# Performance work log

Measured on AMD Instinct MI355X. Metric: run time of the kernel, lower is better.

Reference implementation:

```python
import jax, jax.numpy as jnp
import numpy as np

EPS = 1e-5

def _ln(x):
    m = jnp.mean(x, axis=-1, keepdims=True)
    v = jnp.mean((x - m) ** 2, axis=-1, keepdims=True)
    return (x - m) / jnp.sqrt(v + EPS)

def setup_inputs() -> dict:
    key = jax.random.key(0)
    ks = jax.random.split(key, 6)
    B, S, E, H = 2, 2048, 1024, 16
    sd = 1.0 / np.sqrt(E)
    x = jax.random.normal(ks[0], (B, S, E), dtype=jnp.float32)
    w_in = jax.random.normal(ks[1], (3 * E, E), dtype=jnp.float32) * sd
    w_out = jax.random.normal(ks[2], (E, E), dtype=jnp.float32) * sd
    w_fc = jax.random.normal(ks[3], (4 * E, E), dtype=jnp.float32) * sd
    b_fc = jnp.zeros((4 * E,), dtype=jnp.float32)
    w_proj = jax.random.normal(ks[4], (E, 4 * E), dtype=jnp.float32) * (1.0 / np.sqrt(4 * E))
    b_proj = jnp.zeros((E,), dtype=jnp.float32)
    return {"x": x, "w_in": w_in, "w_out": w_out, "w_fc": w_fc,
            "b_fc": b_fc, "w_proj": w_proj, "b_proj": b_proj}

def reference(x, w_in, w_out, w_fc, b_fc, w_proj, b_proj):
    B, S, E = x.shape
    H = 16
    D = E // H
    h = _ln(x)
    qkv = h @ w_in.T                      # [B,S,3E]
    q, k, v = jnp.split(qkv, 3, axis=-1)
    q = q.reshape(B, S, H, D)
    k = k.reshape(B, S, H, D)
    v = v.reshape(B, S, H, D)
    scale = 1.0 / np.sqrt(D)
    scores = jnp.einsum('bqhd,bkhd->bhqk', q, k) * scale  # [B,H,S,S]
    causal = jnp.tril(jnp.ones((S, S), dtype=bool))
    scores = jnp.where(causal, scores, -jnp.inf)
    attn = jax.nn.softmax(scores, axis=-1)
    o = jnp.einsum('bhqk,bkhd->bqhd', attn, v).reshape(B, S, E)
    attn_out = o @ w_out.T
    x2 = x + attn_out                      # residual 1
    h2 = _ln(x2)
    m = jax.nn.relu(h2 @ w_fc.T + b_fc)    # [B,S,4E]
    return (m @ w_proj.T + b_proj) + x2    # residual 2
```

## Files before the change

### kernel.cpp

```cpp
#include <hip/hip_runtime.h>
#include <stdint.h>

#define AS1 __attribute__((address_space(1)))
#define AS3 __attribute__((address_space(3)))

typedef __bf16 bf8_t __attribute__((ext_vector_type(8)));
typedef float f4_t __attribute__((ext_vector_type(4)));
typedef unsigned short ush;

__device__ __forceinline__ ush f2b(float f) {
  unsigned u = __builtin_bit_cast(unsigned, f);
  u += 0x7fffu + ((u >> 16) & 1u);
  return (ush)(u >> 16);
}
__device__ __forceinline__ void unpack8(uint4 u, float* dst) {
  unsigned a0 = u.x, a1 = u.y, a2 = u.z, a3 = u.w;
  dst[0] = __builtin_bit_cast(float, a0 << 16);
  dst[1] = __builtin_bit_cast(float, a0 & 0xffff0000u);
  dst[2] = __builtin_bit_cast(float, a1 << 16);
  dst[3] = __builtin_bit_cast(float, a1 & 0xffff0000u);
  dst[4] = __builtin_bit_cast(float, a2 << 16);
  dst[5] = __builtin_bit_cast(float, a2 & 0xffff0000u);
  dst[6] = __builtin_bit_cast(float, a3 << 16);
  dst[7] = __builtin_bit_cast(float, a3 & 0xffff0000u);
}

__global__ __launch_bounds__(256) void f2b_all(
    const float* __restrict__ w_in, const float* __restrict__ w_out,
    const float* __restrict__ w_fc, const float* __restrict__ w_proj,
    ush* __restrict__ o_in, ush* __restrict__ o_out,
    ush* __restrict__ o_fc, ush* __restrict__ o_proj) {
  const int blk = blockIdx.x;
  const float* src;
  ush* dst;
  int base;
  if (blk < 3072) { src = w_in; dst = o_in; base = blk; }
  else if (blk < 4096) { src = w_out; dst = o_out; base = blk - 3072; }
  else if (blk < 8192) { src = w_fc; dst = o_fc; base = blk - 4096; }
  else { src = w_proj; dst = o_proj; base = blk - 8192; }
  const int i = (base * 256 + threadIdx.x) * 4;
  float4 v = *(const float4*)(src + i);
  union { ush u[4]; uint2 d; } p;
  p.u[0] = f2b(v.x); p.u[1] = f2b(v.y); p.u[2] = f2b(v.z); p.u[3] = f2b(v.w);
  *(uint2*)(dst + i) = p.d;
}

__global__ __launch_bounds__(256) void ln_kernel(const float* __restrict__ x,
                                                 ush* __restrict__ out) {
  const int row = blockIdx.x, tid = threadIdx.x;
  const float* xr = x + (size_t)row * 1024;
  float4 v = ((const float4*)xr)[tid];
  float s = v.x + v.y + v.z + v.w;
  float q = v.x * v.x + v.y * v.y + v.z * v.z + v.w * v.w;
  for (int o = 32; o; o >>= 1) { s += __shfl_down(s, o); q += __shfl_down(q, o); }
  __shared__ float rs[4], rq[4];
  const int w = tid >> 6;
  if ((tid & 63) == 0) { rs[w] = s; rq[w] = q; }
  __syncthreads();
  s = rs[0] + rs[1] + rs[2] + rs[3];
  q = rq[0] + rq[1] + rq[2] + rq[3];
  const float mean = s * (1.0f / 1024.0f);
  const float var = q * (1.0f / 1024.0f) - mean * mean;
  const float rstd = rsqrtf(var + 1e-5f);
  union { ush u[4]; uint2 d; } p;
  p.u[0] = f2b((v.x - mean) * rstd);
  p.u[1] = f2b((v.y - mean) * rstd);
  p.u[2] = f2b((v.z - mean) * rstd);
  p.u[3] = f2b((v.w - mean) * rstd);
  *(uint2*)(out + (size_t)row * 1024 + tid * 4) = p.d;
}

template <int EPI>
__global__ __launch_bounds__(512, 2) void gemm8p(
    const ush* __restrict__ A, const ush* __restrict__ Bw,
    int M, int N, int K, int lda, int ldb,
    const float* __restrict__ bias, const float* __restrict__ resid,
    float* __restrict__ outF, ush* __restrict__ outB) {
  __shared__ __align__(16) ush lds[65536];
  ush* const LA0 = lds;
  ush* const LA1 = lds + 16384;
  ush* const LB0 = lds + 32768;
  ush* const LB1 = lds + 49152;

  const int tid = threadIdx.x;
  const int wave = tid >> 6, lane = tid & 63;
  const int wm = wave >> 2, wn = wave & 3;
  const int l16 = lane & 15, quad = lane >> 4;
  const int sw = l16 & 7;
  const int bm = blockIdx.x, bn = blockIdx.y;
  const int bmrow = bm * 256, bnrow = bn * 256;
  const size_t kbase = (size_t)blockIdx.z * (size_t)K;
  const int KT = K >> 6;
  const int nit = KT >> 1;
  const int gcs = (((lane & 7) ^ ((lane >> 3) & 7)) << 3);

  auto stage = [&](const ush* __restrict__ gbase, int blkrow, int ld,
                   ush* dstbase, int t, int h) {
    const int kt = t & (KT - 1);
#pragma unroll
    for (int i2 = 0; i2 < 2; ++i2) {
      const int rr = h * 128 + (wave * 2 + i2) * 8 + (lane >> 3);
      const ush* g = gbase + (size_t)(blkrow + rr) * ld + kbase + kt * 64 + gcs;
      __builtin_amdgcn_global_load_lds(
          (const AS1 void*)g,
          (AS3 void*)(dstbase + h * 8192 + (wave * 2 + i2) * 512), 16, 0, 0);
    }
  };

  f4_t acc[8][4];
#pragma unroll
  for (int i = 0; i < 8; ++i)
#pragma unroll
    for (int j = 0; j < 4; ++j) acc[i][j] = (f4_t){0.f, 0.f, 0.f, 0.f};

  stage(A, bmrow, lda, LA0, 0, 0);
  stage(A, bmrow, lda, LA0, 0, 1);
  stage(Bw, bnrow, ldb, LB0, 0, 0);
  stage(Bw, bnrow, ldb, LB0, 0, 1);
  stage(A, bmrow, lda, LA1, 1, 0);
  asm volatile("s_waitcnt vmcnt(2)" ::: "memory");
  __builtin_amdgcn_s_barrier();

  bf8_t af[4][2], bf[2][2];

  for (int it = 0; it < nit; ++it) {
#pragma unroll
    for (int hf = 0; hf < 2; ++hf) {
      ush* const cA = hf ? LA1 : LA0;
      ush* const cB = hf ? LB1 : LB0;
#pragma unroll
      for (int sub = 0; sub < 4; ++sub) {
        const int p = hf * 4 + sub;
        if (sub == 0) {
#pragma unroll
          for (int m = 0; m < 4; ++m)
#pragma unroll
            for (int kk = 0; kk < 2; ++kk)
              af[m][kk] = *(const bf8_t*)&cA[(wm * 128 + m * 16 + l16) * 64 +
                                            (((kk * 4 + quad) ^ sw) << 3)];
#pragma unroll
          for (int n = 0; n < 2; ++n)
#pragma unroll
            for (int kk = 0; kk < 2; ++kk)
              bf[n][kk] = *(const bf8_t*)&cB[(wn * 64 + n * 16 + l16) * 64 +
                                            (((kk * 4 + quad) ^ sw) << 3)];
        } else if (sub == 1) {
#pragma unroll
          for (int n = 0; n < 2; ++n)
#pragma unroll
            for (int kk = 0; kk < 2; ++kk)
              bf[n][kk] = *(const bf8_t*)&cB[(wn * 64 + (2 + n) * 16 + l16) * 64 +
                                            (((kk * 4 + quad) ^ sw) << 3)];
        } else if (sub == 2) {
#pragma unroll
          for (int m = 0; m < 4; ++m)
#pragma unroll
            for (int kk = 0; kk < 2; ++kk)
              af[m][kk] = *(const bf8_t*)&cA[(wm * 128 + (4 + m) * 16 + l16) * 64 +
                                            (((kk * 4 + quad) ^ sw) << 3)];
#pragma unroll
          for (int n = 0; n < 2; ++n)
#pragma unroll
            for (int kk = 0; kk < 2; ++kk)
              bf[n][kk] = *(const bf8_t*)&cB[(wn * 64 + n * 16 + l16) * 64 +
                                            (((kk * 4 + quad) ^ sw) << 3)];
        } else {
#pragma unroll
          for (int n = 0; n < 2; ++n)
#pragma unroll
            for (int kk = 0; kk < 2; ++kk)
              bf[n][kk] = *(const bf8_t*)&cB[(wn * 64 + (2 + n) * 16 + l16) * 64 +
                                            (((kk * 4 + quad) ^ sw) << 3)];
        }
        if (p == 0) stage(A, bmrow, lda, LA1, 2 * it + 1, 1);
        else if (p == 1) stage(Bw, bnrow, ldb, LB1, 2 * it + 1, 0);
        else if (p == 2) stage(Bw, bnrow, ldb, LB1, 2 * it + 1, 1);
        else if (p == 3) stage(A, bmrow, lda, LA0, 2 * it + 2, 0);
        else if (p == 4) stage(A, bmrow, lda, LA0, 2 * it + 2, 1);
        else if (p == 5) stage(Bw, bnrow, ldb, LB0, 2 * it + 2, 0);
        else if (p == 6) stage(Bw, bnrow, ldb, LB0, 2 * it + 2, 1);
        else stage(A, bmrow, lda, LA1, 2 * it + 3, 0);
        if (sub == 3) asm volatile("s_waitcnt vmcnt(2)" ::: "memory");
        __builtin_amdgcn_s_barrier();
        asm volatile("s_waitcnt lgkmcnt(0)" ::: "memory");
        __builtin_amdgcn_sched_barrier(0);
        __builtin_amdgcn_s_setprio(1);
        const int mo = (sub >= 2) ? 4 : 0;
        const int no = (sub & 1) ? 2 : 0;
#pragma unroll
        for (int m = 0; m < 4; ++m)
#pragma unroll
          for (int n = 0; n < 2; ++n)
#pragma unroll
            for (int kk = 0; kk < 2; ++kk)
              acc[mo + m][no + n] = __builtin_amdgcn_mfma_f32_16x16x32_bf16(
                  af[m][kk], bf[n][kk], acc[mo + m][no + n], 0, 0, 0);
        __builtin_amdgcn_s_setprio(0);
        __builtin_amdgcn_s_barrier();
      }
    }
  }

  asm volatile("s_waitcnt vmcnt(0)" ::: "memory");
  __builtin_amdgcn_s_barrier();

  if (EPI == 0 || EPI == 2) {
    ush* outBz = outB + (size_t)blockIdx.z * ((size_t)M * N);
    ush* eb = lds + wave * 8192;
    float bv[4];
    if (EPI == 2) {
#pragma unroll
      for (int ni = 0; ni < 4; ++ni) bv[ni] = bias[bn * 256 + wn * 64 + ni * 16 + l16];
    }
#pragma unroll
    for (int mi = 0; mi < 8; ++mi)
#pragma unroll
      for (int ni = 0; ni < 4; ++ni)
#pragma unroll
        for (int r = 0; r < 4; ++r) {
          float v = acc[mi][ni][r];
          if (EPI == 2) v = fmaxf(v + bv[ni], 0.0f);
          eb[(mi * 16 + quad * 4 + r) * 64 + ni * 16 + l16] = f2b(v);
        }
    asm volatile("s_waitcnt lgkmcnt(0)" ::: "memory");
#pragma unroll
    for (int j = 0; j < 16; ++j) {
      const int lr = j * 8 + (lane >> 3);
      const int c8 = (lane & 7) * 8;
      uint4 v = *(const uint4*)&eb[lr * 64 + c8];
      *(uint4*)(outBz + (size_t)(bm * 256 + wm * 128 + lr) * N + bn * 256 +
                wn * 64 + c8) = v;
    }
  } else {
#pragma unroll
    for (int mi = 0; mi < 8; ++mi)
#pragma unroll
      for (int ni = 0; ni < 4; ++ni) {
        const int gm0 = bm * 256 + wm * 128 + mi * 16 + quad * 4;
        const int gn = bn * 256 + wn * 64 + ni * 16 + l16;
        const float bv = (EPI == 3) ? bias[gn] : 0.0f;
#pragma unroll
        for (int r = 0; r < 4; ++r) {
          const size_t idx = (size_t)(gm0 + r) * N + gn;
          outF[idx] = acc[mi][ni][r] + bv + resid[idx];
        }
      }
  }
}

__global__ __launch_bounds__(256) void reduce4(const ush* __restrict__ p,
                                               const float* __restrict__ bias,
                                               const float* __restrict__ resid,
                                               float* __restrict__ out) {
  const size_t i = ((size_t)blockIdx.x * 256 + threadIdx.x) * 8;
  const int col = (int)(i & 1023);
  float acc[8];
  float4 r0 = *(const float4*)(resid + i);
  float4 r1 = *(const float4*)(resid + i + 4);
  acc[0] = r0.x + bias[col + 0]; acc[1] = r0.y + bias[col + 1];
  acc[2] = r0.z + bias[col + 2]; acc[3] = r0.w + bias[col + 3];
  acc[4] = r1.x + bias[col + 4]; acc[5] = r1.y + bias[col + 5];
  acc[6] = r1.z + bias[col + 6]; acc[7] = r1.w + bias[col + 7];
#pragma unroll
  for (int z = 0; z < 4; ++z) {
    uint4 u = *(const uint4*)(p + (size_t)z * 4194304 + i);
    float f[8]; unpack8(u, f);
#pragma unroll
    for (int j = 0; j < 8; ++j) acc[j] += f[j];
  }
  *(float4*)(out + i) = *(float4*)acc;
  *(float4*)(out + i + 4) = *(float4*)(acc + 4);
}

template <int EPI, int BM, int MINW>
__global__ __launch_bounds__(256, MINW) void gemm_bt(
    const ush* __restrict__ A, const ush* __restrict__ Bw,
    int M, int N, int K,
    const float* __restrict__ bias, const float* __restrict__ resid,
    float* __restrict__ outF, ush* __restrict__ outB) {
  constexpr int MI = BM / 32;
  constexpr int NCH = (BM + 128) / 16;
  constexpr int PC = NCH / 4;
  constexpr int ASZ = BM * 32;
  __shared__ ush lds[2 * ASZ + 2 * 4096];
  const int tid = threadIdx.x;
  const int wave = tid >> 6, lane = tid & 63;
  const int bm = blockIdx.x, bn = blockIdx.y;
  const int wm = (wave & 1) * (BM / 2), wn = (wave >> 1) * 64;
  const int l16 = lane & 15, quad = lane >> 4;
  const int srow = lane >> 2;
  const int scol = (lane & 3) * 8;

  const ush* Abase = A + (size_t)(bm * BM) * K;
  const ush* Bbase = Bw + (size_t)(bn * 128) * K;

  f4_t acc[MI][4];
#pragma unroll
  for (int i = 0; i < MI; ++i)
#pragma unroll
    for (int j = 0; j < 4; ++j) acc[i][j] = (f4_t){0.f, 0.f, 0.f, 0.f};

  const int kiters = K >> 5;

  auto stage = [&](int k0, int buf) {
    const int kk = k0 * 32;
#pragma unroll
    for (int i = 0; i < PC; ++i) {
      const int c = wave * PC + i;
      if (c < BM / 16) {
        const ush* ga = Abase + (size_t)(c * 16 + srow) * K + kk + scol;
        __builtin_amdgcn_global_load_lds((const AS1 void*)ga,
                                         (AS3 void*)(lds + buf * ASZ + c * 512), 16, 0, 0);
      } else {
        const int c2 = c - BM / 16;
        const ush* gb = Bbase + (size_t)(c2 * 16 + srow) * K + kk + scol;
        __builtin_amdgcn_global_load_lds(
            (const AS1 void*)gb, (AS3 void*)(lds + 2 * ASZ + buf * 4096 + c2 * 512), 16, 0, 0);
      }
    }
  };

  stage(0, 0);
  __syncthreads();
  for (int k0 = 0; k0 < kiters; ++k0) {
    const int cur = k0 & 1;
    if (k0 + 1 < kiters) stage(k0 + 1, cur ^ 1);
    bf8_t af[MI], bfr[4];
#pragma unroll
    for (int mi = 0; mi < MI; ++mi)
      af[mi] = *(const bf8_t*)&lds[cur * ASZ + (wm + mi * 16 + l16) * 32 + quad * 8];
#pragma unroll
    for (int ni = 0; ni < 4; ++ni)
      bfr[ni] = *(const bf8_t*)&lds[2 * ASZ + cur * 4096 + (wn + ni * 16 + l16) * 32 + quad * 8];
#pragma unroll
    for (int mi = 0; mi < MI; ++mi)
#pragma unroll
      for (int ni = 0; ni < 4; ++ni)
        acc[mi][ni] =
            __builtin_amdgcn_mfma_f32_16x16x32_bf16(af[mi], bfr[ni], acc[mi][ni], 0, 0, 0);
    __syncthreads();
  }

  if (EPI == 0 || EPI == 2) {
    ush* eb = lds + wave * ASZ;
#pragma unroll
    for (int mi = 0; mi < MI; ++mi)
#pragma unroll
      for (int ni = 0; ni < 4; ++ni) {
        const int gn = bn * 128 + wn + ni * 16 + l16;
        const float bv = (EPI == 2) ? bias[gn] : 0.0f;
#pragma unroll
        for (int r = 0; r < 4; ++r) {
          float v = acc[mi][ni][r] + bv;
          if (EPI == 2) v = fmaxf(v, 0.0f);
          eb[(mi * 16 + quad * 4 + r) * 64 + ni * 16 + l16] = f2b(v);
        }
      }
#pragma unroll
    for (int j = 0; j < BM / 16; ++j) {
      const int lr = j * 8 + (lane >> 3);
      const int c8 = (lane & 7) * 8;
      uint4 v = *(const uint4*)&eb[lr * 64 + c8];
      *(uint4*)(outB + (size_t)(bm * BM + wm + lr) * N + bn * 128 + wn + c8) = v;
    }
  } else {
#pragma unroll
    for (int mi = 0; mi < MI; ++mi) {
#pragma unroll
      for (int ni = 0; ni < 4; ++ni) {
        const int gm0 = bm * BM + wm + mi * 16 + quad * 4;
        const int gn = bn * 128 + wn + ni * 16 + l16;
        const float bv = (EPI == 3) ? bias[gn] : 0.0f;
#pragma unroll
        for (int r = 0; r < 4; ++r) {
          const size_t idx = (size_t)(gm0 + r) * N + gn;
          outF[idx] = acc[mi][ni][r] + bv + resid[idx];
        }
      }
    }
  }
}

__global__ __launch_bounds__(256) void pack_kv(const ush* __restrict__ qkv,
                                               ush* __restrict__ Kp,
                                               ush* __restrict__ Vp) {
  const int lin = blockIdx.x;
  const int kt = lin & 31, h = (lin >> 5) & 15, b = lin >> 9;
  const int tid = threadIdx.x;
  __shared__ ush Vs[64 * 72];
  const size_t rowbase = (size_t)(b * 2048 + kt * 64) * 3072 + h * 64;
  ush* Kt = Kp + (size_t)lin * 4096;
  ush* Vt = Vp + (size_t)lin * 4096;

  const int r0 = tid >> 3, cin = tid & 7;
#pragma unroll
  for (int it = 0; it < 2; ++it) {
    const int r = r0 + it * 32;
    uint4 ku = *(const uint4*)(qkv + rowbase + (size_t)r * 3072 + 1024 + cin * 8);
    float f[8]; unpack8(ku, f);
    union { ush us[8]; uint4 v; } pk;
#pragma unroll
    for (int j = 0; j < 8; ++j) pk.us[j] = f2b(f[j] * 0.18033688f);
    *(uint4*)(Kt + (size_t)(r * 8 + (cin ^ (r & 7))) * 8) = pk.v;
    uint4 vu = *(const uint4*)(qkv + rowbase + (size_t)r * 3072 + 2048 + cin * 8);
    *(uint4*)&Vs[r * 72 + cin * 8] = vu;
  }
  __syncthreads();
#pragma unroll
  for (int oc2 = 0; oc2 < 2; ++oc2) {
    const int oc = tid * 2 + oc2;
    const int d = oc >> 3, c = oc & 7;
    const int k0 = 8 * (c ^ (d & 7));
    union { ush us[8]; uint4 v; } pk;
#pragma unroll
    for (int j = 0; j < 8; ++j) pk.us[j] = Vs[(k0 + j) * 72 + d];
    *(uint4*)(Vt + (size_t)oc * 8) = pk.v;
  }
}

__global__ __launch_bounds__(256, 4) void attn_kernel(const ush* __restrict__ qkv,
                                                      const ush* __restrict__ Kp,
                                                      const ush* __restrict__ Vp,
                                                      ush* __restrict__ o) {
  const int lin = blockIdx.x;
  const int b = lin & 1, h = (lin >> 1) & 15, tq = 31 - (lin >> 5);
  const int tid = threadIdx.x;
  const int wave = tid >> 6, lane = tid & 63;
  const int l15 = lane & 15, quad = lane >> 4;

  __shared__ __align__(16) ush Ks[2 * 4096];
  __shared__ __align__(16) ush Vt[2 * 4096];
  __shared__ __align__(16) ush Ps[64 * 72];

  bf8_t qf[2];
  {
    const int qrow = b * 2048 + tq * 64 + wave * 16 + l15;
#pragma unroll
    for (int s = 0; s < 2; ++s) {
      union { uint4 u; bf8_t v; } pk;
      pk.u = *(const uint4*)(qkv + (size_t)qrow * 3072 + h * 64 + s * 32 + quad * 8);
      qf[s] = pk.v;
    }
  }

  float m_s = -1e30f, l_s = 0.f;
  f4_t O[4];
#pragma unroll
  for (int j = 0; j < 4; ++j) O[j] = (f4_t){0.f, 0.f, 0.f, 0.f};

  const int qw0 = tq * 64 + wave * 16;
  const int swz = (l15 & 7) * 8;
  const size_t tile0 = (size_t)((b * 16 + h) * 32) * 4096;

  {
    const ush* Ktile = Kp + tile0;
    const ush* Vtile = Vp + tile0;
#pragma unroll
    for (int i = 0; i < 2; ++i) {
      const int seg = wave * 2 + i;
      __builtin_amdgcn_global_load_lds((const AS1 void*)(Ktile + seg * 512 + lane * 8),
                                       (AS3 void*)(Ks + seg * 512), 16, 0, 0);
      __builtin_amdgcn_global_load_lds((const AS1 void*)(Vtile + seg * 512 + lane * 8),
                                       (AS3 void*)(Vt + seg * 512), 16, 0, 0);
    }
  }
  asm volatile("s_waitcnt vmcnt(0)" ::: "memory");
  __builtin_amdgcn_s_barrier();

  for (int kt = 0; kt <= tq; ++kt) {
    const int cur = (kt & 1) * 4096;
    const int nxt = 4096 - cur;
    if (kt < tq) {
      const ush* Ktile = Kp + tile0 + (size_t)(kt + 1) * 4096;
      const ush* Vtile = Vp + tile0 + (size_t)(kt + 1) * 4096;
#pragma unroll
      for (int i = 0; i < 2; ++i) {
        const int seg = wave * 2 + i;
        __builtin_amdgcn_global_load_lds((const AS1 void*)(Ktile + seg * 512 + lane * 8),
                                         (AS3 void*)(Ks + nxt + seg * 512), 16, 0, 0);
        __builtin_amdgcn_global_load_lds((const AS1 void*)(Vtile + seg * 512 + lane * 8),
                                         (AS3 void*)(Vt + nxt + seg * 512), 16, 0, 0);
      }
    }

    f4_t S[4];
#pragma unroll
    for (int mi = 0; mi < 4; ++mi) S[mi] = (f4_t){0.f, 0.f, 0.f, 0.f};
#pragma unroll
    for (int s = 0; s < 2; ++s)
#pragma unroll
      for (int mi = 0; mi < 4; ++mi) {
        bf8_t kf = *(const bf8_t*)&Ks[cur + (mi * 16 + l15) * 64 + (((4 * s + quad) * 8) ^ swz)];
        S[mi] = __builtin_amdgcn_mfma_f32_16x16x32_bf16(kf, qf[s], S[mi], 0, 0, 0);
      }

    if (kt == tq) {
#pragma unroll
      for (int mi = 0; mi < 4; ++mi)
#pragma unroll
        for (int r = 0; r < 4; ++r) {
          const int kg = kt * 64 + mi * 16 + quad * 4 + r;
          const int qg = qw0 + l15;
          if (kg > qg) S[mi][r] = -1e30f;
        }
    }

    float mx = -1e30f;
#pragma unroll
    for (int mi = 0; mi < 4; ++mi)
#pragma unroll
      for (int r = 0; r < 4; ++r) mx = fmaxf(mx, S[mi][r]);
    mx = fmaxf(mx, __shfl_xor(mx, 16));
    mx = fmaxf(mx, __shfl_xor(mx, 32));

    if (!__all(mx - m_s <= 8.0f)) {
      const float mn = fmaxf(m_s, mx);
      const float dm = m_s - mn;
      float alpha;
      asm("v_exp_f32 %0, %1" : "=v"(alpha) : "v"(dm));
      float ar[4];
#pragma unroll
      for (int r = 0; r < 4; ++r) ar[r] = __shfl(alpha, quad * 4 + r);
#pragma unroll
      for (int n4 = 0; n4 < 4; ++n4)
#pragma unroll
        for (int r = 0; r < 4; ++r) O[n4][r] *= ar[r];
      l_s *= alpha;
      m_s = mn;
    }

    float sum = 0.f;
#pragma unroll
    for (int mi = 0; mi < 4; ++mi)
#pragma unroll
      for (int r = 0; r < 4; ++r) {
        const float z = S[mi][r] - m_s;
        float pv;
        asm("v_exp_f32 %0, %1" : "=v"(pv) : "v"(z));
        S[mi][r] = pv;
        sum += pv;
      }
    sum += __shfl_xor(sum, 16);
    sum += __shfl_xor(sum, 32);
    l_s += sum;

#pragma unroll
    for (int mi = 0; mi < 4; ++mi) {
      uint2 w2;
      asm("v_cvt_pk_bf16_f32 %0, %1, %2" : "=v"(w2.x) : "v"(S[mi][0]), "v"(S[mi][1]));
      asm("v_cvt_pk_bf16_f32 %0, %1, %2" : "=v"(w2.y) : "v"(S[mi][2]), "v"(S[mi][3]));
      *(uint2*)&Ps[(wave * 16 + l15) * 72 + mi * 16 + quad * 4] = w2;
    }

    bf8_t pf[2], vf[4][2];
#pragma unroll
    for (int s = 0; s < 2; ++s)
      pf[s] = *(const bf8_t*)&Ps[(wave * 16 + l15) * 72 + s * 32 + quad * 8];
#pragma unroll
    for (int n4 = 0; n4 < 4; ++n4)
#pragma unroll
      for (int s = 0; s < 2; ++s)
        vf[n4][s] = *(const bf8_t*)&Vt[cur + (n4 * 16 + l15) * 64 + (((4 * s + quad) * 8) ^ swz)];
#pragma unroll
    for (int n4 = 0; n4 < 4; ++n4)
#pragma unroll
      for (int s = 0; s < 2; ++s)
        O[n4] = __builtin_amdgcn_mfma_f32_16x16x32_bf16(pf[s], vf[n4][s], O[n4], 0, 0, 0);

    asm volatile("s_waitcnt vmcnt(0)" ::: "memory");
    __builtin_amdgcn_s_barrier();
  }

  const float rc = 1.0f / l_s;
  float rr[4];
#pragma unroll
  for (int r = 0; r < 4; ++r) rr[r] = __shfl(rc, quad * 4 + r);
#pragma unroll
  for (int n4 = 0; n4 < 4; ++n4)
#pragma unroll
    for (int r = 0; r < 4; ++r) {
      const int qg = tq * 64 + wave * 16 + quad * 4 + r;
      o[(size_t)(b * 2048 + qg) * 1024 + h * 64 + n4 * 16 + l15] = f2b(O[n4][r] * rr[r]);
    }
}

extern "C" void kernel_launch(void* const* d_in, const int* in_sizes, int n_in,
                              void* d_out, int out_size, void* d_ws, size_t ws_size,
                              hipStream_t stream) {
  const float* x = (const float*)d_in[0];
  const float* w_in = (const float*)d_in[1];
  const float* w_out = (const float*)d_in[2];
  const float* w_fc = (const float*)d_in[3];
  const float* b_fc = (const float*)d_in[4];
  const float* w_proj = (const float*)d_in[5];
  const float* b_proj = (const float*)d_in[6];
  float* out = (float*)d_out;

  char* ws = (char*)d_ws;
  ush* w_in_b = (ush*)(ws);
  ush* w_out_b = (ush*)(ws + 6291456);
  ush* h_b = (ush*)(ws + 8388608);
  ush* Kp = (ush*)(ws + 16777216);
  ush* Vp = (ush*)(ws + 25165824);
  ush* Pp = (ush*)(ws);
  ush* w_fc_b = (ush*)(ws + 33554432);
  ush* w_proj_b = (ush*)(ws + 41943040);
  float* x2 = (float*)(ws + 50331648);
  ush* qkv_b = (ush*)(ws + 67108864);
  ush* m_b = (ush*)(ws + 67108864);
  ush* o_b = (ush*)(ws + 92274688);

  f2b_all<<<12288, 256, 0, stream>>>(w_in, w_out, w_fc, w_proj,
                                     w_in_b, w_out_b, w_fc_b, w_proj_b);

  ln_kernel<<<4096, 256, 0, stream>>>(x, h_b);

  gemm8p<0><<<dim3(16, 12), 512, 0, stream>>>(
      h_b, w_in_b, 4096, 3072, 1024, 1024, 1024, nullptr, nullptr, nullptr, qkv_b);

  pack_kv<<<1024, 256, 0, stream>>>(qkv_b, Kp, Vp);

  attn_kernel<<<1024, 256, 0, stream>>>(qkv_b, Kp, Vp, o_b);

  gemm_bt<1, 64, 4><<<dim3(64, 8), 256, 0, stream>>>(
      o_b, w_out_b, 4096, 1024, 1024, nullptr, x, x2, nullptr);

  ln_kernel<<<4096, 256, 0, stream>>>(x2, h_b);

  gemm8p<2><<<dim3(16, 16), 512, 0, stream>>>(
      h_b, w_fc_b, 4096, 4096, 1024, 1024, 1024, b_fc, nullptr, nullptr, m_b);

  gemm8p<0><<<dim3(16, 4, 4), 512, 0, stream>>>(
      m_b, w_proj_b, 4096, 1024, 1024, 4096, 4096, nullptr, nullptr, nullptr, Pp);

  reduce4<<<2048, 256, 0, stream>>>(Pp, b_proj, x2, out);
}
```

Baseline: 303.5 us.

## Rebalance causal attention block order, swizzle P tile, defer row-sum reduction

Reorders the query-tile assignment so neighbouring blocks alternate long and short causal rows, which is meant to balance work across CUs. It also replaces the padded P shared-memory layout with an XOR swizzle, hoists the V fragment loads ahead of the QK MFMAs, and wraps both MFMA groups in s_setprio. The per-tile cross-lane row-sum shuffles are moved out of the loop into a single reduction at the end. Together these aim to cut tail imbalance, LDS footprint and per-iteration shuffle latency, at the cost of holding the V fragments in registers for longer.

After: 298.4 us. Within noise of the previous version (-1.7%).

```diff
diff --git a/kernel.cpp b/kernel.cpp
--- a/kernel.cpp
+++ b/kernel.cpp
@@ -423,14 +423,19 @@
                                                       const ush* __restrict__ Vp,
                                                       ush* __restrict__ o) {
   const int lin = blockIdx.x;
-  const int b = lin & 1, h = (lin >> 1) & 15, tq = 31 - (lin >> 5);
+  const int b = lin & 1, h = (lin >> 1) & 15;
+  const int sg = lin >> 5, jg = sg >> 3, kg = sg & 7;
+  const int tq = (jg == 0) ? (31 - 2 * kg)
+               : (jg == 1) ? (2 * kg)
+               : (jg == 2) ? (30 - 2 * kg)
+                           : (2 * kg + 1);
   const int tid = threadIdx.x;
   const int wave = tid >> 6, lane = tid & 63;
   const int l15 = lane & 15, quad = lane >> 4;
 
   __shared__ __align__(16) ush Ks[2 * 4096];
   __shared__ __align__(16) ush Vt[2 * 4096];
-  __shared__ __align__(16) ush Ps[64 * 72];
+  __shared__ __align__(16) ush Ps[64 * 64];
 
   bf8_t qf[2];
   {
@@ -443,13 +448,15 @@
     }
   }
 
-  float m_s = -1e30f, l_s = 0.f;
+  float m_s = -1e30f, l_part = 0.f;
   f4_t O[4];
 #pragma unroll
   for (int j = 0; j < 4; ++j) O[j] = (f4_t){0.f, 0.f, 0.f, 0.f};
 
   const int qw0 = tq * 64 + wave * 16;
   const int swz = (l15 & 7) * 8;
+  const int prow = wave * 16 + l15;
+  const int pswz = (prow & 7) << 3;
   const size_t tile0 = (size_t)((b * 16 + h) * 32) * 4096;
 
   {
@@ -483,9 +490,17 @@
       }
     }
 
+    bf8_t vf[4][2];
+#pragma unroll
+    for (int n4 = 0; n4 < 4; ++n4)
+#pragma unroll
+      for (int s = 0; s < 2; ++s)
+        vf[n4][s] = *(const bf8_t*)&Vt[cur + (n4 * 16 + l15) * 64 + (((4 * s + quad) * 8) ^ swz)];
+
     f4_t S[4];
 #pragma unroll
     for (int mi = 0; mi < 4; ++mi) S[mi] = (f4_t){0.f, 0.f, 0.f, 0.f};
+    __builtin_amdgcn_s_setprio(1);
 #pragma unroll
     for (int s = 0; s < 2; ++s)
 #pragma unroll
@@ -493,23 +508,24 @@
         bf8_t kf = *(const bf8_t*)&Ks[cur + (mi * 16 + l15) * 64 + (((4 * s + quad) * 8) ^ swz)];
         S[mi] = __builtin_amdgcn_mfma_f32_16x16x32_bf16(kf, qf[s], S[mi], 0, 0, 0);
       }
+    __builtin_amdgcn_s_setprio(0);
 
     if (kt == tq) {
 #pragma unroll
       for (int mi = 0; mi < 4; ++mi)
 #pragma unroll
         for (int r = 0; r < 4; ++r) {
-          const int kg = kt * 64 + mi * 16 + quad * 4 + r;
+          const int kg2 = kt * 64 + mi * 16 + quad * 4 + r;
           const int qg = qw0 + l15;
-          if (kg > qg) S[mi][r] = -1e30f;
+          if (kg2 > qg) S[mi][r] = -1e30f;
         }
     }
 
-    float mx = -1e30f;
-#pragma unroll
-    for (int mi = 0; mi < 4; ++mi)
-#pragma unroll
-      for (int r = 0; r < 4; ++r) mx = fmaxf(mx, S[mi][r]);
+    float t0 = fmaxf(fmaxf(S[0][0], S[0][1]), fmaxf(S[0][2], S[0][3]));
+    float t1 = fmaxf(fmaxf(S[1][0], S[1][1]), fmaxf(S[1][2], S[1][3]));
+    float t2 = fmaxf(fmaxf(S[2][0], S[2][1]), fmaxf(S[2][2], S[2][3]));
+    float t3 = fmaxf(fmaxf(S[3][0], S[3][1]), fmaxf(S[3][2], S[3][3]));
+    float mx = fmaxf(fmaxf(t0, t1), fmaxf(t2, t3));
     mx = fmaxf(mx, __shfl_xor(mx, 16));
     mx = fmaxf(mx, __shfl_xor(mx, 32));
 
@@ -525,7 +541,7 @@
       for (int n4 = 0; n4 < 4; ++n4)
 #pragma unroll
         for (int r = 0; r < 4; ++r) O[n4][r] *= ar[r];
-      l_s *= alpha;
+      l_part *= alpha;
       m_s = mn;
     }
 
@@ -540,37 +556,35 @@
         S[mi][r] = pv;
         sum += pv;
       }
-    sum += __shfl_xor(sum, 16);
-    sum += __shfl_xor(sum, 32);
-    l_s += sum;
+    l_part += sum;
 
 #pragma unroll
     for (int mi = 0; mi < 4; ++mi) {
       uint2 w2;
       asm("v_cvt_pk_bf16_f32 %0, %1, %2" : "=v"(w2.x) : "v"(S[mi][0]), "v"(S[mi][1]));
       asm("v_cvt_pk_bf16_f32 %0, %1, %2" : "=v"(w2.y) : "v"(S[mi][2]), "v"(S[mi][3]));
-      *(uint2*)&Ps[(wave * 16 + l15) * 72 + mi * 16 + quad * 4] = w2;
-    }
-
-    bf8_t pf[2], vf[4][2];
+      *(uint2*)&Ps[prow * 64 + ((mi * 16 + quad * 4) ^ pswz)] = w2;
+    }
+
+    bf8_t pf[2];
 #pragma unroll
     for (int s = 0; s < 2; ++s)
-      pf[s] = *(const bf8_t*)&Ps[(wave * 16 + l15) * 72 + s * 32 + quad * 8];
-#pragma unroll
-    for (int n4 = 0; n4 < 4; ++n4)
-#pragma unroll
-      for (int s = 0; s < 2; ++s)
-        vf[n4][s] = *(const bf8_t*)&Vt[cur + (n4 * 16 + l15) * 64 + (((4 * s + quad) * 8) ^ swz)];
+      pf[s] = *(const bf8_t*)&Ps[prow * 64 + ((s * 32 + quad * 8) ^ pswz)];
+    __builtin_amdgcn_s_setprio(1);
 #pragma unroll
     for (int n4 = 0; n4 < 4; ++n4)
 #pragma unroll
       for (int s = 0; s < 2; ++s)
         O[n4] = __builtin_amdgcn_mfma_f32_16x16x32_bf16(pf[s], vf[n4][s], O[n4], 0, 0, 0);
+    __builtin_amdgcn_s_setprio(0);
 
     asm volatile("s_waitcnt vmcnt(0)" ::: "memory");
     __builtin_amdgcn_s_barrier();
   }
 
+  float l_s = l_part;
+  l_s += __shfl_xor(l_s, 16);
+  l_s += __shfl_xor(l_s, 32);
   const float rc = 1.0f / l_s;
   float rr[4];
 #pragma unroll
```
